# Kernel tuning notes

Measured on AMD Instinct MI355X. Metric: run time of the kernel, lower is better.

## Reference

```python
import jax, jax.numpy as jnp
from jax import lax
import numpy as np

DIM = 64
NUM_HEADS = 1
SR_RATIO = 8
LN_EPS = 1e-3  # Keras LayerNormalization default


def setup_inputs() -> dict:
    key = jax.random.key(0)
    ks = jax.random.split(key, 8)
    B, H, W = 8, 128, 128
    N, C = H * W, DIM
    s = 0.02
    x = jax.random.normal(ks[0], (B, N, C), dtype=jnp.float32)
    Wq = jax.random.normal(ks[1], (C, C), dtype=jnp.float32) * s
    Wkv = jax.random.normal(ks[2], (C, 2 * C), dtype=jnp.float32) * s
    sr_kernel = jax.random.normal(ks[3], (SR_RATIO, SR_RATIO, C, C), dtype=jnp.float32) * s
    sr_bias = jnp.zeros((C,), dtype=jnp.float32)
    ln_gamma = jnp.ones((C,), dtype=jnp.float32)
    ln_beta = jnp.zeros((C,), dtype=jnp.float32)
    Wproj = jax.random.normal(ks[4], (C, C), dtype=jnp.float32) * s
    bproj = jnp.zeros((C,), dtype=jnp.float32)
    return {"x": x, "H": H, "W": W, "Wq": Wq, "Wkv": Wkv,
            "sr_kernel": sr_kernel, "sr_bias": sr_bias,
            "ln_gamma": ln_gamma, "ln_beta": ln_beta,
            "Wproj": Wproj, "bproj": bproj}


def reference(x, H, W, Wq, Wkv, sr_kernel, sr_bias, ln_gamma, ln_beta, Wproj, bproj):
    B, N, C = x.shape
    nh = NUM_HEADS
    hd = C // nh
    scale = hd ** -0.5

    # q: [B, nh, N, hd]
    q = (x @ Wq).reshape(B, N, nh, hd).transpose(0, 2, 1, 3)

    # spatial-reduction KV path (faithful to the TF code, incl. its
    # transpose-then-reshape ordering)
    x_ = jnp.transpose(x, (0, 2, 1)).reshape(B, H, W, C)
    x_ = lax.conv_general_dilated(
        x_, sr_kernel, window_strides=(SR_RATIO, SR_RATIO), padding="VALID",
        dimension_numbers=("NHWC", "HWIO", "NHWC")) + sr_bias
    M = x_.shape[1] * x_.shape[2]
    x_ = x_.reshape(B, M, C)
    # LayerNorm over last axis
    mu = jnp.mean(x_, axis=-1, keepdims=True)
    var = jnp.mean(jnp.square(x_ - mu), axis=-1, keepdims=True)
    x_ = (x_ - mu) * lax.rsqrt(var + LN_EPS) * ln_gamma + ln_beta

    kv = (x_ @ Wkv).reshape(B, M, 2, nh, hd).transpose(2, 0, 3, 1, 4)
    k, v = kv[0], kv[1]  # [B, nh, M, hd]

    attn = jax.nn.softmax(jnp.einsum("bhnd,bhmd->bhnm", q, k) * scale, axis=-1)
    out = jnp.einsum("bhnm,bhmd->bhnd", attn, v)
    out = out.transpose(0, 2, 1, 3).reshape(B, N, C)
    return out @ Wproj + bproj
```

## Files before the change

### kernel.cpp

```cpp
#include <hip/hip_runtime.h>
#include <hip/hip_bf16.h>

#define B_   8
#define N_   16384
#define C_   64
#define M_   256
#define NPB  1048576

typedef __attribute__((ext_vector_type(8))) short short8v;
typedef __attribute__((ext_vector_type(16))) float f32x16;
typedef __attribute__((ext_vector_type(4)))  float f32x4;

union FragU { short8v s8; unsigned u[4]; };

__device__ inline unsigned pkbf(float a, float b) {
  union { __hip_bfloat162 h2; unsigned u; } cv;
  cv.h2 = __float22bfloat162_rn(make_float2(a, b));
  return cv.u;
}
__device__ inline unsigned short bfbits(float a) {
  union { __hip_bfloat16 h; unsigned short u; } cv;
  cv.h = __float2bfloat16(a);
  return cv.u;
}
__device__ inline float bf2f(unsigned short u) {
  union { unsigned u; float f; } cv;
  cv.u = ((unsigned)u) << 16;
  return cv.f;
}
__device__ inline short8v ld8(const unsigned short* p) {
  return *(const short8v*)p;
}

__device__ inline void plswap(unsigned &a, unsigned &b) {
#if __has_builtin(__builtin_amdgcn_permlane32_swap)
  typedef unsigned uint2v __attribute__((ext_vector_type(2)));
  uint2v r = __builtin_amdgcn_permlane32_swap(a, b, false, false);
  a = r[0]; b = r[1];
#else
  asm volatile("v_permlane32_swap_b32 %0, %1" : "+v"(a), "+v"(b));
#endif
}

__device__ inline void repack16(const f32x16 s, FragU& f0, FragU& f1) {
  #pragma unroll
  for (int h = 0; h < 2; ++h) {
    FragU& f = h ? f1 : f0;
    unsigned a0 = pkbf(s[8*h+0], s[8*h+1]);
    unsigned a1 = pkbf(s[8*h+2], s[8*h+3]);
    unsigned a2 = pkbf(s[8*h+4], s[8*h+5]);
    unsigned a3 = pkbf(s[8*h+6], s[8*h+7]);
    plswap(a0, a2);
    plswap(a1, a3);
    f.u[0] = a0; f.u[1] = a1; f.u[2] = a2; f.u[3] = a3;
  }
}

__global__ __launch_bounds__(256) void prep(const float* __restrict__ Wq,
                                            const float* __restrict__ Wp,
                                            const float* __restrict__ Kw,
                                            const float* __restrict__ Wkv,
                                            unsigned short* __restrict__ kbt,
                                            float* __restrict__ wkp,
                                            float* __restrict__ wvp) {
  const int gi = blockIdx.x;
  if (gi < 1024) {
    const int idx = gi * 256 + threadIdx.x;
    const int j = idx & 7, l = (idx >> 3) & 63, s = (idx >> 9) & 15;
    const int w = (idx >> 13) & 3, kw = idx >> 15;
    const int e = s * 32 + 8 * (l >> 4) + j;
    const int par = e >> 8, ci = (e >> 2) & 63, jj = e & 3;
    const int kh = 2 * jj + par, co = 16 * w + (l & 15);
    kbt[idx] = bfbits(Kw[(size_t)((kh * 8 + kw) * 64 + ci) * 64 + co]);
  } else {
    const int idx = (gi - 1024) * 256 + threadIdx.x;
    const int c = idx & 63, cc = (idx >> 6) & 63, sel = idx >> 12;
    float s = 0.f;
    if (sel == 0) {
      #pragma unroll 8
      for (int d = 0; d < 64; ++d) s += Wkv[cc * 128 + d] * Wq[c * 64 + d];
      wkp[cc * 64 + c] = s * 0.125f * 1.4426950408889634f;
    } else {
      #pragma unroll 8
      for (int d = 0; d < 64; ++d) s += Wkv[cc * 128 + 64 + d] * Wp[d * 64 + c];
      wvp[cc * 64 + c] = s;
    }
  }
}

__global__ __launch_bounds__(256) void conv_mfma(const float* __restrict__ x,
                                                 const unsigned short* __restrict__ kbt,
                                                 unsigned short* __restrict__ xrb) {
  const int kw = blockIdx.x & 7;
  const int ow = (blockIdx.x >> 3) & 15;
  const int b  = blockIdx.x >> 7;
  const int t  = threadIdx.x, w = t >> 6, l = t & 63;
  const int oh = l & 15, kg = l >> 4;

  const float* xb = x + (size_t)b * NPB + (size_t)((ow * 8 + kw) * 64) * 64 + oh * 4;
  const unsigned short* kb = kbt + (size_t)(((kw * 4 + w) * 16) * 64 + l) * 8;

  f32x4 acc = {0.f, 0.f, 0.f, 0.f};
  #pragma unroll
  for (int s = 0; s < 16; ++s) {
    const int par = (s >= 8) ? 1 : 0;
    const int ci  = ((s * 8) + kg * 2) & 63;
    const float* ax = xb + (size_t)par * 524288 + ci * 64;
    const float4 a0 = *(const float4*)(ax);
    const float4 a1 = *(const float4*)(ax + 64);
    FragU af;
    af.u[0] = pkbf(a0.x, a0.y); af.u[1] = pkbf(a0.z, a0.w);
    af.u[2] = pkbf(a1.x, a1.y); af.u[3] = pkbf(a1.z, a1.w);
    const short8v bfrag = ld8(kb + s * 512);
    acc = __builtin_amdgcn_mfma_f32_16x16x32_bf16(af.s8, bfrag, acc, 0, 0, 0);
  }
  unsigned short* dst = xrb + (size_t)kw * 131072
                      + ((size_t)b * 256 + ow) * 64 + w * 16 + (l & 15);
  #pragma unroll
  for (int r = 0; r < 4; ++r)
    dst[(size_t)((l >> 4) * 4 + r) * 1024] = bfbits(acc[r]);
}

__global__ __launch_bounds__(256) void ln_kv(const unsigned short* __restrict__ xrb,
                                             const float* __restrict__ sr_bias,
                                             const float* __restrict__ gamma,
                                             const float* __restrict__ beta,
                                             const float* __restrict__ wkp,
                                             const float* __restrict__ wvp,
                                             unsigned short* __restrict__ kbl,
                                             unsigned short* __restrict__ vbl) {
  const int w   = threadIdx.x >> 6;
  const int row = blockIdx.x * 4 + w;
  const int c   = threadIdx.x & 63;
  float val = sr_bias[c];
  #pragma unroll
  for (int s = 0; s < 8; ++s)
    val += bf2f(xrb[(size_t)s * 131072 + (size_t)row * 64 + c]);

  float sum = val;
  #pragma unroll
  for (int off = 32; off; off >>= 1) sum += __shfl_xor(sum, off, 64);
  const float mu = sum * (1.f / 64.f);
  const float d  = val - mu;
  float vs = d * d;
  #pragma unroll
  for (int off = 32; off; off >>= 1) vs += __shfl_xor(vs, off, 64);
  const float rs = rsqrtf(vs * (1.f / 64.f) + 1e-3f);
  const float ln = d * rs * gamma[c] + beta[c];

  __shared__ float lnrow[4][64];
  lnrow[w][c] = ln;
  __syncthreads();

  float ka = 0.f, va = 0.f;
  #pragma unroll 8
  for (int cc = 0; cc < 64; ++cc) {
    const float l = lnrow[w][cc];
    ka += l * wkp[cc * 64 + c];
    va += l * wvp[cc * 64 + c];
  }
  const int m = row & 255, bb = row >> 8;
  kbl[(size_t)bb * 16384
      + (size_t)((((m >> 5) * 4 + (c >> 4)) * 64) + (m & 31) + 32 * ((c >> 3) & 1)) * 8
      + (c & 7)] = bfbits(ka);
  vbl[(size_t)bb * 16384
      + (size_t)(((c >> 5) * 8 + (m >> 5)) * 2 + ((m >> 4) & 1)) * 512
      + (size_t)((c & 31) + 32 * ((m >> 3) & 1)) * 8
      + (m & 7)] = bfbits(va);
}

__global__ __launch_bounds__(512, 4) void attn_mfma(const float* __restrict__ x,
                                                    const unsigned short* __restrict__ kbl,
                                                    const unsigned short* __restrict__ vbl,
                                                    const float* __restrict__ bp,
                                                    float* __restrict__ out) {
  __shared__ char smem[65536];
  unsigned short* ks = (unsigned short*)smem;
  unsigned short* vs = ks + 16384;
  const int t    = threadIdx.x;
  const int w    = t >> 6;
  const int l    = t & 63;
  const int l31  = l & 31;
  const int hi   = l >> 5;
  const int b    = blockIdx.x >> 6;
  const int tile = blockIdx.x & 63;
  const size_t nrow = (size_t)b * N_ + (size_t)tile * 256;
  const int qloc = w * 32 + l31;

  {
    typedef __attribute__((ext_vector_type(2))) unsigned long long ull2;
    const ull2* kg = (const ull2*)(kbl + (size_t)b * 16384);
    const ull2* vg = (const ull2*)(vbl + (size_t)b * 16384);
    ull2* kd = (ull2*)ks;
    ull2* vd = (ull2*)vs;
    #pragma unroll
    for (int i = 0; i < 4; ++i) {
      kd[i * 512 + t] = kg[i * 512 + t];
      vd[i * 512 + t] = vg[i * 512 + t];
    }
  }

  const float* xrow = x + (nrow + qloc) * 64;
  FragU xb[4];
  #pragma unroll
  for (int tt = 0; tt < 4; ++tt) {
    const float* p = xrow + 16 * tt + 8 * hi;
    const float4 x0 = *(const float4*)(p);
    const float4 x1 = *(const float4*)(p + 4);
    xb[tt].u[0] = pkbf(x0.x, x0.y); xb[tt].u[1] = pkbf(x0.z, x0.w);
    xb[tt].u[2] = pkbf(x1.x, x1.y); xb[tt].u[3] = pkbf(x1.z, x1.w);
  }
  __syncthreads();

  const unsigned short* kfp = ks + l * 8;
  const unsigned short* vfp = vs + l * 8;
  f32x16 Z;
  #pragma unroll
  for (int r = 0; r < 16; ++r) Z[r] = 0.f;
  f32x16 O0 = Z, O1 = Z;
  float ss = 0.f;

  #pragma unroll
  for (int kt = 0; kt < 8; ++kt) {
    const short8v vf00 = ld8(vfp + (size_t)((kt * 2 + 0) * 512));
    const short8v vf01 = ld8(vfp + (size_t)((kt * 2 + 1) * 512));
    const short8v vf10 = ld8(vfp + (size_t)(((8 + kt) * 2 + 0) * 512));
    const short8v vf11 = ld8(vfp + (size_t)(((8 + kt) * 2 + 1) * 512));
    f32x16 S = __builtin_amdgcn_mfma_f32_32x32x16_bf16(
        ld8(kfp + (size_t)((kt * 4 + 0) * 512)), xb[0].s8, Z, 0, 0, 0);
    #pragma unroll
    for (int tt = 1; tt < 4; ++tt) {
      const short8v ak = ld8(kfp + (size_t)((kt * 4 + tt) * 512));
      S = __builtin_amdgcn_mfma_f32_32x32x16_bf16(ak, xb[tt].s8, S, 0, 0, 0);
    }
    f32x16 P;
    #pragma unroll
    for (int r = 0; r < 16; ++r) {
      const float pv = exp2f(S[r]);
      P[r] = pv; ss += pv;
    }
    FragU f0, f1;
    repack16(P, f0, f1);
    O0 = __builtin_amdgcn_mfma_f32_32x32x16_bf16(vf00, f0.s8, O0, 0, 0, 0);
    O0 = __builtin_amdgcn_mfma_f32_32x32x16_bf16(vf01, f1.s8, O0, 0, 0, 0);
    O1 = __builtin_amdgcn_mfma_f32_32x32x16_bf16(vf10, f0.s8, O1, 0, 0, 0);
    O1 = __builtin_amdgcn_mfma_f32_32x32x16_bf16(vf11, f1.s8, O1, 0, 0, 0);
  }

  ss += __shfl_xor(ss, 32);
  const float inv = 1.f / ss;

  float* ot = (float*)smem;
  __syncthreads();

  #pragma unroll
  for (int ph = 0; ph < 2; ++ph) {
    if ((w >> 2) == ph) {
      const int slot = (w & 3) * 32 + l31;
      #pragma unroll
      for (int g = 0; g < 4; ++g) {
        const int co0 = 8 * g + 4 * hi, co1 = 32 + 8 * g + 4 * hi;
        const float4 b0 = *(const float4*)(bp + co0);
        const float4 b1 = *(const float4*)(bp + co1);
        *(float4*)&ot[slot * 68 + co0] =
            make_float4(O0[4*g+0]*inv + b0.x, O0[4*g+1]*inv + b0.y,
                        O0[4*g+2]*inv + b0.z, O0[4*g+3]*inv + b0.w);
        *(float4*)&ot[slot * 68 + co1] =
            make_float4(O1[4*g+0]*inv + b1.x, O1[4*g+1]*inv + b1.y,
                        O1[4*g+2]*inv + b1.z, O1[4*g+3]*inv + b1.w);
      }
    }
    __syncthreads();
    float4* out4 = (float4*)(out + (nrow + ph * 128) * 64);
    #pragma unroll
    for (int i = 0; i < 4; ++i) {
      const int idx = i * 512 + t;
      const int row = idx >> 4, c4 = idx & 15;
      out4[idx] = *(const float4*)&ot[row * 68 + c4 * 4];
    }
    __syncthreads();
  }
}

extern "C" void kernel_launch(void* const* d_in, const int* in_sizes, int n_in,
                              void* d_out, int out_size, void* d_ws, size_t ws_size,
                              hipStream_t stream) {
  const float* x   = (const float*)d_in[0];
  const float* Wq  = (const float*)d_in[3];
  const float* Wkv = (const float*)d_in[4];
  const float* Kw  = (const float*)d_in[5];
  const float* sb  = (const float*)d_in[6];
  const float* gam = (const float*)d_in[7];
  const float* bet = (const float*)d_in[8];
  const float* Wp  = (const float*)d_in[9];
  const float* bp  = (const float*)d_in[10];
  float* out = (float*)d_out;

  unsigned short* xrb = (unsigned short*)d_ws;
  unsigned short* kbl = xrb + 1048576;
  unsigned short* vbl = kbl + 131072;
  unsigned short* kbt = vbl + 131072;
  float* wkp = (float*)(kbt + 262144);
  float* wvp = wkp + 4096;

  prep<<<1056, 256, 0, stream>>>(Wq, Wp, Kw, Wkv, kbt, wkp, wvp);
  conv_mfma<<<1024, 256, 0, stream>>>(x, kbt, xrb);
  ln_kv<<<512, 256, 0, stream>>>(xrb, sb, gam, bet, wkp, wvp, kbl, vbl);
  attn_mfma<<<512, 512, 0, stream>>>(x, kbl, vbl, bp, out);
}
```

Baseline: 47.86 us.

## Split attention keys across two waves and prefetch conv inputs in register batches

The attention kernel now runs 128-thread blocks, each covering 32 queries. The two waves each handle half of the 256 keys, reading K/V fragments straight from global memory instead of staging them in LDS. Partial outputs and softmax sums are combined through a small shared buffer. Separately, the conv kernel double-buffers its strided input loads in groups of four so global latency overlaps with MFMA work. The cost is redundant K/V global reads per small block, served from cache, plus an extra reduction step.

```diff
diff --git a/kernel.cpp b/kernel.cpp
--- a/kernel.cpp
+++ b/kernel.cpp
@@ -100,20 +100,43 @@
   const float* xb = x + (size_t)b * NPB + (size_t)((ow * 8 + kw) * 64) * 64 + oh * 4;
   const unsigned short* kb = kbt + (size_t)(((kw * 4 + w) * 16) * 64 + l) * 8;
 
+  #define CONV_ADDR(s) (xb + (size_t)(((s) >= 8) ? 1 : 0) * 524288 \
+                           + ((((s) * 8) + kg * 2) & 63) * 64)
+
+  float4 A0[8], A1[8];
   f32x4 acc = {0.f, 0.f, 0.f, 0.f};
-  #pragma unroll
-  for (int s = 0; s < 16; ++s) {
-    const int par = (s >= 8) ? 1 : 0;
-    const int ci  = ((s * 8) + kg * 2) & 63;
-    const float* ax = xb + (size_t)par * 524288 + ci * 64;
-    const float4 a0 = *(const float4*)(ax);
-    const float4 a1 = *(const float4*)(ax + 64);
-    FragU af;
-    af.u[0] = pkbf(a0.x, a0.y); af.u[1] = pkbf(a0.z, a0.w);
-    af.u[2] = pkbf(a1.x, a1.y); af.u[3] = pkbf(a1.z, a1.w);
-    const short8v bfrag = ld8(kb + s * 512);
-    acc = __builtin_amdgcn_mfma_f32_16x16x32_bf16(af.s8, bfrag, acc, 0, 0, 0);
-  }
+
+  #pragma unroll
+  for (int i = 0; i < 4; ++i) {
+    const float* ax = CONV_ADDR(i);
+    A0[2 * i]     = *(const float4*)(ax);
+    A0[2 * i + 1] = *(const float4*)(ax + 64);
+  }
+  #pragma unroll
+  for (int g = 0; g < 4; ++g) {
+    if (g < 3) {
+      #pragma unroll
+      for (int i = 0; i < 4; ++i) {
+        const int s2 = (g + 1) * 4 + i;
+        const float* ax = CONV_ADDR(s2);
+        if ((g & 1) == 0) { A1[2*i] = *(const float4*)(ax); A1[2*i+1] = *(const float4*)(ax + 64); }
+        else              { A0[2*i] = *(const float4*)(ax); A0[2*i+1] = *(const float4*)(ax + 64); }
+      }
+    }
+    #pragma unroll
+    for (int i = 0; i < 4; ++i) {
+      const int s = g * 4 + i;
+      const float4 a0 = ((g & 1) == 0) ? A0[2*i]   : A1[2*i];
+      const float4 a1 = ((g & 1) == 0) ? A0[2*i+1] : A1[2*i+1];
+      FragU af;
+      af.u[0] = pkbf(a0.x, a0.y); af.u[1] = pkbf(a0.z, a0.w);
+      af.u[2] = pkbf(a1.x, a1.y); af.u[3] = pkbf(a1.z, a1.w);
+      const short8v bfrag = ld8(kb + s * 512);
+      acc = __builtin_amdgcn_mfma_f32_16x16x32_bf16(af.s8, bfrag, acc, 0, 0, 0);
+    }
+  }
+  #undef CONV_ADDR
+
   unsigned short* dst = xrb + (size_t)kw * 131072
                       + ((size_t)b * 256 + ow) * 64 + w * 16 + (l & 15);
   #pragma unroll
@@ -169,38 +192,23 @@
       + (m & 7)] = bfbits(va);
 }
 
-__global__ __launch_bounds__(512, 4) void attn_mfma(const float* __restrict__ x,
+__global__ __launch_bounds__(128, 6) void attn_mfma(const float* __restrict__ x,
                                                     const unsigned short* __restrict__ kbl,
                                                     const unsigned short* __restrict__ vbl,
                                                     const float* __restrict__ bp,
                                                     float* __restrict__ out) {
-  __shared__ char smem[65536];
-  unsigned short* ks = (unsigned short*)smem;
-  unsigned short* vs = ks + 16384;
+  __shared__ float comb[64 * 33];
+  __shared__ float ot[32 * 68];
   const int t    = threadIdx.x;
   const int w    = t >> 6;
   const int l    = t & 63;
   const int l31  = l & 31;
   const int hi   = l >> 5;
-  const int b    = blockIdx.x >> 6;
-  const int tile = blockIdx.x & 63;
-  const size_t nrow = (size_t)b * N_ + (size_t)tile * 256;
-  const int qloc = w * 32 + l31;
-
-  {
-    typedef __attribute__((ext_vector_type(2))) unsigned long long ull2;
-    const ull2* kg = (const ull2*)(kbl + (size_t)b * 16384);
-    const ull2* vg = (const ull2*)(vbl + (size_t)b * 16384);
-    ull2* kd = (ull2*)ks;
-    ull2* vd = (ull2*)vs;
-    #pragma unroll
-    for (int i = 0; i < 4; ++i) {
-      kd[i * 512 + t] = kg[i * 512 + t];
-      vd[i * 512 + t] = vg[i * 512 + t];
-    }
-  }
-
-  const float* xrow = x + (nrow + qloc) * 64;
+  const int b    = blockIdx.x >> 9;
+  const int tile = blockIdx.x & 511;
+  const size_t nrow = (size_t)b * N_ + (size_t)tile * 32;
+
+  const float* xrow = x + (nrow + l31) * 64;
   FragU xb[4];
   #pragma unroll
   for (int tt = 0; tt < 4; ++tt) {
@@ -210,10 +218,9 @@
     xb[tt].u[0] = pkbf(x0.x, x0.y); xb[tt].u[1] = pkbf(x0.z, x0.w);
     xb[tt].u[2] = pkbf(x1.x, x1.y); xb[tt].u[3] = pkbf(x1.z, x1.w);
   }
-  __syncthreads();
-
-  const unsigned short* kfp = ks + l * 8;
-  const unsigned short* vfp = vs + l * 8;
+
+  const unsigned short* kfp = kbl + (size_t)b * 16384 + l * 8;
+  const unsigned short* vfp = vbl + (size_t)b * 16384 + l * 8;
   f32x16 Z;
   #pragma unroll
   for (int r = 0; r < 16; ++r) Z[r] = 0.f;
@@ -221,7 +228,8 @@
   float ss = 0.f;
 
   #pragma unroll
-  for (int kt = 0; kt < 8; ++kt) {
+  for (int ki = 0; ki < 4; ++ki) {
+    const int kt = w * 4 + ki;
     const short8v vf00 = ld8(vfp + (size_t)((kt * 2 + 0) * 512));
     const short8v vf01 = ld8(vfp + (size_t)((kt * 2 + 1) * 512));
     const short8v vf10 = ld8(vfp + (size_t)(((8 + kt) * 2 + 0) * 512));
@@ -247,38 +255,41 @@
     O1 = __builtin_amdgcn_mfma_f32_32x32x16_bf16(vf11, f1.s8, O1, 0, 0, 0);
   }
 
-  ss += __shfl_xor(ss, 32);
-  const float inv = 1.f / ss;
-
-  float* ot = (float*)smem;
+  if (w == 1) {
+    float* dst = comb + l * 33;
+    #pragma unroll
+    for (int r = 0; r < 16; ++r) { dst[r] = O0[r]; dst[16 + r] = O1[r]; }
+    dst[32] = ss;
+  }
   __syncthreads();
-
-  #pragma unroll
-  for (int ph = 0; ph < 2; ++ph) {
-    if ((w >> 2) == ph) {
-      const int slot = (w & 3) * 32 + l31;
-      #pragma unroll
-      for (int g = 0; g < 4; ++g) {
-        const int co0 = 8 * g + 4 * hi, co1 = 32 + 8 * g + 4 * hi;
-        const float4 b0 = *(const float4*)(bp + co0);
-        const float4 b1 = *(const float4*)(bp + co1);
-        *(float4*)&ot[slot * 68 + co0] =
-            make_float4(O0[4*g+0]*inv + b0.x, O0[4*g+1]*inv + b0.y,
-                        O0[4*g+2]*inv + b0.z, O0[4*g+3]*inv + b0.w);
-        *(float4*)&ot[slot * 68 + co1] =
-            make_float4(O1[4*g+0]*inv + b1.x, O1[4*g+1]*inv + b1.y,
-                        O1[4*g+2]*inv + b1.z, O1[4*g+3]*inv + b1.w);
-      }
-    }
-    __syncthreads();
-    float4* out4 = (float4*)(out + (nrow + ph * 128) * 64);
-    #pragma unroll
-    for (int i = 0; i < 4; ++i) {
-      const int idx = i * 512 + t;
-      const int row = idx >> 4, c4 = idx & 15;
-      out4[idx] = *(const float4*)&ot[row * 68 + c4 * 4];
-    }
-    __syncthreads();
+  if (w == 0) {
+    const float* src = comb + l * 33;
+    #pragma unroll
+    for (int r = 0; r < 16; ++r) { O0[r] += src[r]; O1[r] += src[16 + r]; }
+    ss += src[32];
+    ss += __shfl_xor(ss, 32);
+    const float inv = 1.f / ss;
+    #pragma unroll
+    for (int g = 0; g < 4; ++g) {
+      const int co0 = 8 * g + 4 * hi, co1 = 32 + 8 * g + 4 * hi;
+      const float4 b0 = *(const float4*)(bp + co0);
+      const float4 b1 = *(const float4*)(bp + co1);
+      *(float4*)&ot[l31 * 68 + co0] =
+          make_float4(O0[4*g+0]*inv + b0.x, O0[4*g+1]*inv + b0.y,
+                      O0[4*g+2]*inv + b0.z, O0[4*g+3]*inv + b0.w);
+      *(float4*)&ot[l31 * 68 + co1] =
+          make_float4(O1[4*g+0]*inv + b1.x, O1[4*g+1]*inv + b1.y,
+                      O1[4*g+2]*inv + b1.z, O1[4*g+3]*inv + b1.w);
+    }
+  }
+  __syncthreads();
+
+  float4* out4 = (float4*)(out + nrow * 64);
+  #pragma unroll
+  for (int i = 0; i < 4; ++i) {
+    const int idx = i * 128 + t;
+    const int row = idx >> 4, c4 = idx & 15;
+    out4[idx] = *(const float4*)&ot[row * 68 + c4 * 4];
   }
 }
 
@@ -306,5 +317,5 @@
   prep<<<1056, 256, 0, stream>>>(Wq, Wp, Kw, Wkv, kbt, wkp, wvp);
   conv_mfma<<<1024, 256, 0, stream>>>(x, kbt, xrb);
   ln_kv<<<512, 256, 0, stream>>>(xrb, sb, gam, bet, wkp, wvp, kbl, vbl);
-  attn_mfma<<<512, 512, 0, stream>>>(x, kbl, vbl, bp, out);
-}
+  attn_mfma<<<4096, 128, 0, stream>>>(x, kbl, vbl, bp, out);
+}
```

Result: slower. 57.27 us (+19.7%).
